# Kernel tuning notes

Hardware: AMD Instinct MI355X
Metric: run time of the kernel (lower is better)

Reference implementation:

```python
import jax, jax.numpy as jnp
import numpy as np

B, T, D, C = 16, 2048, 512, 20
K_EASY, K_HARD = 40, 20
M_BIG, M_SMALL = 7, 3
A4 = A5 = A6 = A7 = 1.0
EPS = 1e-05
DROP_P = 0.6


def setup_inputs() -> dict:
    key = jax.random.key(0)
    ks = jax.random.split(key, 6)
    attn = jax.random.uniform(ks[0], (B, T, 1), dtype=jnp.float32)
    mu = jax.random.normal(ks[1], (B, T, D), dtype=jnp.float32)
    var = jax.random.uniform(ks[2], (B, T, D), dtype=jnp.float32) * 0.9 + 0.1
    mu_clip = jax.random.normal(ks[3], (B, T, D), dtype=jnp.float32)
    text_feat = jax.random.normal(ks[4], (C, D), dtype=jnp.float32)
    keep = (jax.random.uniform(ks[5], (B, T)) >= DROP_P).astype(jnp.float32)
    drop_mask = keep / (1.0 - DROP_P)  # inverted-dropout mask on a ones tensor
    return dict(attn=attn, mu=mu, var=var, mu_clip=mu_clip, text_feat=text_feat, drop_mask=drop_mask)


def _normalize(x, axis=-1):
    n = jnp.linalg.norm(x, axis=axis, keepdims=True)
    return x / jnp.maximum(n, 1e-12)


def _select_topk(scores, emb, k):
    # torch: sort desc, take first k indices, gather along time dim
    _, idx = jax.lax.top_k(scores, k)  # [B,k]
    return jnp.take_along_axis(emb, idx[:, :, None], axis=1)  # [B,k,D]


def _window_reduce(x, w, op_min):
    # binary erosion/dilation along time with structure ones((1,w)), border_value=0
    lo, hi = w // 2, w - 1 - w // 2
    xp = jnp.pad(x, ((0, 0), (lo, hi)), constant_values=0.0)
    if op_min:
        return jax.lax.reduce_window(xp, jnp.inf, jax.lax.min, (1, w), (1, 1), 'VALID')
    return jax.lax.reduce_window(xp, -jnp.inf, jax.lax.max, (1, w), (1, 1), 'VALID')


def _kl_distance(mu_p, cov_p, mu_q, cov_q):
    # vectorized over all (i in k_p) x (j in k_q) pairs
    cov_p = cov_p + EPS
    cov_q = cov_q + EPS
    d = mu_p.shape[-1]
    diff = mu_q[:, None, :, :] - mu_p[:, :, None, :]        # [B,kp,kq,D]
    term1 = 0.5 * jnp.sum(diff * diff / cov_q[:, None, :, :], axis=-1)
    term2 = 0.5 * (jnp.sum(jnp.log(cov_q), -1)[:, None, :] - jnp.sum(jnp.log(cov_p), -1)[:, :, None])
    term3 = 0.5 * jnp.sum(cov_p[:, :, None, :] / cov_q[:, None, :, :], axis=-1)
    dist = term1 + term2 + term3 - 0.5 * d
    return jnp.mean(1.0 / (dist + 1.0), axis=(1, 2))        # [B]


def _prob_contrastive(hard_q, easy_pos, easy_neg):
    pos = _kl_distance(hard_q[0], hard_q[1], easy_pos[0], easy_pos[1])
    neg = _kl_distance(hard_q[0], hard_q[1], easy_neg[0], easy_neg[1])
    return jnp.mean(-(jnp.log(pos) + jnp.log(1.0 - neg)))


def _forward(attn, mu, var, mu_clip, text_feat, drop_mask):
    a = attn[..., 0]                                        # [B,T]
    a_drop = a * drop_mask
    a_rev = jnp.max(a, axis=1, keepdims=True) - a
    a_rev_drop = a_rev * drop_mask
    easy_act = (_select_topk(a_drop, mu, K_EASY), _select_topk(a_drop, var, K_EASY))
    easy_bkg = (_select_topk(a_rev_drop, mu, K_EASY), _select_topk(a_rev_drop, var, K_EASY))

    med = jnp.median(a, axis=1, keepdims=True)
    abin = jnp.where(a > med, 1.0, 0.0)
    er_M = _window_reduce(abin, M_BIG, True)
    er_m = _window_reduce(abin, M_SMALL, True)
    inner = jax.lax.stop_gradient(er_m - er_M)              # mask computed on detached numpy in torch
    dl_m = _window_reduce(abin, M_SMALL, False)
    dl_M = _window_reduce(abin, M_BIG, False)
    outer = jax.lax.stop_gradient(dl_M - dl_m)
    a_inner = a * inner
    a_outer = a * outer
    hard_act = (_select_topk(a_inner, mu, K_HARD), _select_topk(a_inner, var, K_HARD))
    hard_bkg = (_select_topk(a_outer, mu, K_HARD), _select_topk(a_outer, var, K_HARD))

    # Distillation
    sim = jnp.einsum('btd,btd->bt', _normalize(mu), _normalize(mu_clip))
    distill = A4 * (-jnp.log(jnp.mean((sim + 1.0) / 2.0)))

    act_loss = A5 * _prob_contrastive(hard_act, easy_act, easy_bkg)
    bkg_loss = A6 * _prob_contrastive(hard_bkg, easy_bkg, easy_act)

    emb = _normalize(text_feat)
    sim_m = emb @ jax.lax.stop_gradient(emb.T) - jnp.eye(emb.shape[0], dtype=emb.dtype)
    ortho = A7 * jnp.linalg.norm(sim_m)

    total = distill + act_loss + bkg_loss + ortho
    return total, distill, act_loss, bkg_loss, ortho


def reference(attn, mu, var, mu_clip, text_feat, drop_mask):
    return _forward(attn, mu, var, mu_clip, text_feat, drop_mask)
```

## Files before the change

kernel.cpp:

```cpp
#include <hip/hip_runtime.h>
#include <math.h>


#define BB 16
#define TT 2048
#define DD 512
#define CC 20
#define KEASY 40
#define KHARD 20
#define EPSF 1e-5f

typedef unsigned long long u64;

template <int CTRL>
__device__ __forceinline__ float dpp_mov(float x) {
  return __int_as_float(__builtin_amdgcn_update_dpp(
      0, __float_as_int(x), CTRL, 0xF, 0xF, true));
}
__device__ __forceinline__ float wsum63(float v) {
  v += dpp_mov<0x111>(v);
  v += dpp_mov<0x112>(v);
  v += dpp_mov<0x114>(v);
  v += dpp_mov<0x118>(v);
  v += dpp_mov<0x142>(v);
  v += dpp_mov<0x143>(v);
  return v;
}
__device__ __forceinline__ float wsum_bc(float v) {
  return __int_as_float(__builtin_amdgcn_readlane(__float_as_int(wsum63(v)), 63));
}
__device__ __forceinline__ float wmax_bc(float v) {
  v = fmaxf(v, dpp_mov<0x111>(v));
  v = fmaxf(v, dpp_mov<0x112>(v));
  v = fmaxf(v, dpp_mov<0x114>(v));
  v = fmaxf(v, dpp_mov<0x118>(v));
  v = fmaxf(v, dpp_mov<0x142>(v));
  v = fmaxf(v, dpp_mov<0x143>(v));
  return __int_as_float(__builtin_amdgcn_readlane(__float_as_int(v), 63));
}

__device__ __forceinline__ float kth_val(const float (&v)[32], unsigned k, unsigned hi) {
  unsigned lo = 0;
  while (lo < hi) {
    const unsigned mid = lo + ((hi - lo + 1) >> 1);
    const float mf = __uint_as_float(mid);
    unsigned c = 0;
#pragma unroll
    for (int r = 0; r < 32; r++) c += (unsigned)__popcll(__ballot(v[r] >= mf));
    if (c >= k) lo = mid; else hi = mid - 1;
  }
  return __uint_as_float(lo);
}

__global__ __launch_bounds__(256) void k_main1(const float* __restrict__ attn,
                                               const float* __restrict__ drop,
                                               const float* __restrict__ mu,
                                               const float* __restrict__ muc,
                                               const float* __restrict__ var,
                                               int* __restrict__ idxb,
                                               float* __restrict__ slogb,
                                               float* __restrict__ part,
                                               double* __restrict__ acc) {
  const int tid = threadIdx.x, wid = tid >> 6, lane = tid & 63;

  if (blockIdx.x >= 64) {
    __shared__ float s_red[4];
    const int blk = blockIdx.x - 64;
    const float* pmu = mu + (size_t)(blk * 4 + wid) * DD + lane * 4;
    const float* pmc = muc + (size_t)(blk * 4 + wid) * DD + lane * 4;
    float4 xa = *(const float4*)(pmu);
    float4 xb = *(const float4*)(pmu + 256);
    float4 ya = *(const float4*)(pmc);
    float4 yb = *(const float4*)(pmc + 256);
    float wacc = 0.f;
#pragma unroll
    for (int it = 0; it < 4; it++) {
      const float4 cxa = xa, cxb = xb, cya = ya, cyb = yb;
      if (it < 3) {
        const size_t off = (size_t)(it + 1) * 8192 * DD;
        xa = *(const float4*)(pmu + off);
        xb = *(const float4*)(pmu + off + 256);
        ya = *(const float4*)(pmc + off);
        yb = *(const float4*)(pmc + off + 256);
      }
      float dot = 0.f, n1 = 0.f, n2 = 0.f;
      dot = fmaf(cxa.x, cya.x, fmaf(cxa.y, cya.y, fmaf(cxa.z, cya.z, fmaf(cxa.w, cya.w, dot))));
      n1 = fmaf(cxa.x, cxa.x, fmaf(cxa.y, cxa.y, fmaf(cxa.z, cxa.z, fmaf(cxa.w, cxa.w, n1))));
      n2 = fmaf(cya.x, cya.x, fmaf(cya.y, cya.y, fmaf(cya.z, cya.z, fmaf(cya.w, cya.w, n2))));
      dot = fmaf(cxb.x, cyb.x, fmaf(cxb.y, cyb.y, fmaf(cxb.z, cyb.z, fmaf(cxb.w, cyb.w, dot))));
      n1 = fmaf(cxb.x, cxb.x, fmaf(cxb.y, cxb.y, fmaf(cxb.z, cxb.z, fmaf(cxb.w, cxb.w, n1))));
      n2 = fmaf(cyb.x, cyb.x, fmaf(cyb.y, cyb.y, fmaf(cyb.z, cyb.z, fmaf(cyb.w, cyb.w, n2))));
      dot = wsum63(dot);
      n1 = wsum63(n1);
      n2 = wsum63(n2);
      if (lane == 63) {
        const float sim = dot / (fmaxf(sqrtf(n1), 1e-12f) * fmaxf(sqrtf(n2), 1e-12f));
        wacc += (sim + 1.0f) * 0.5f;
      }
    }
    if (lane == 63) s_red[wid] = wacc;
    __syncthreads();
    if (tid == 0) part[blk] = s_red[0] + s_red[1] + s_red[2] + s_red[3];
    return;
  }

  __shared__ float s_a[TT];
  __shared__ int s_idx[KEASY];
  const int b = blockIdx.x >> 2, sel = blockIdx.x & 3;
  for (int i = tid; i < TT; i += 256) s_a[i] = attn[b * TT + i];
  __syncthreads();

  if (tid < 64) {
    if (blockIdx.x == 0) acc[lane] = 0.0;
    float v[32];
    float med = 0.f, mx = 0.f;
    if (sel >= 2) {
#pragma unroll
      for (int r = 0; r < 32; r++) v[r] = s_a[r * 64 + lane];
      const float v1 = kth_val(v, 1024, 0x3F800000u);
      const float v2 = kth_val(v, 1025, __float_as_uint(v1));
      med = 0.5f * (v1 + v2);
    }
    if (sel == 1) {
      float m = 0.f;
#pragma unroll
      for (int r = 0; r < 32; r++) m = fmaxf(m, s_a[r * 64 + lane]);
      mx = wmax_bc(m);
    }
#pragma unroll
    for (int r = 0; r < 32; r++) {
      const int i = r * 64 + lane;
      const float a = s_a[i];
      float score;
      if (sel == 0) {
        score = a * drop[b * TT + i];
      } else if (sel == 1) {
        score = (mx - a) * drop[b * TT + i];
      } else {
        bool sall = true, ball = true, sany = false, bany = false;
#pragma unroll
        for (int o = -3; o <= 3; o++) {
          const int t = i + o;
          const bool one = (t >= 0 && t < TT) ? (s_a[t] > med) : false;
          if (o >= -1 && o <= 1) { sall = sall && one; sany = sany || one; }
          ball = ball && one;
          bany = bany || one;
        }
        score = (sel == 2) ? ((sall && !ball) ? a : 0.f)
                           : ((bany && !sany) ? a : 0.f);
      }
      v[r] = score;
    }
    const unsigned K = (sel < 2) ? KEASY : KHARD;
    const unsigned hiS = (sel < 2) ? 0x40200000u : 0x3F800000u;
    const float ss = kth_val(v, K, hiS);
    unsigned cgt = 0;
#pragma unroll
    for (int r = 0; r < 32; r++) cgt += (unsigned)__popcll(__ballot(v[r] > ss));
    unsigned need = K - cgt;
    unsigned base = 0;
    const u64 lmask = (1ull << lane) - 1;
    int* dst = idxb + sel * (BB * KEASY) + b * KEASY;
#pragma unroll
    for (int r = 0; r < 32; r++) {
      const bool gt = v[r] > ss;
      const bool eq = v[r] == ss;
      const u64 beq = __ballot(eq);
      const unsigned neq = (unsigned)__popcll(beq);
      const unsigned take = (need < neq) ? need : neq;
      const bool tk = eq && ((unsigned)__popcll(beq & lmask) < take);
      const u64 bsel = __ballot(gt || tk);
      if (gt || tk) {
        const unsigned pos = base + (unsigned)__popcll(bsel & lmask);
        dst[pos] = r * 64 + lane;
        s_idx[pos] = r * 64 + lane;
      }
      base += (unsigned)__popcll(bsel);
      need -= take;
    }
  }
  __syncthreads();

  const int Ksel = (sel < 2) ? KEASY : KHARD;
  for (int j = wid; j < Ksel; j += 4) {
    const int t = s_idx[j];
    const float* row = var + ((size_t)b * TT + t) * DD;
    float a2 = 0.f;
#pragma unroll
    for (int c = 0; c < 2; c++) {
      float4 vv = *(const float4*)(row + c * 256 + lane * 4);
      a2 += __logf(vv.x + EPSF) + __logf(vv.y + EPSF) +
            __logf(vv.z + EPSF) + __logf(vv.w + EPSF);
    }
    a2 = wsum63(a2);
    if (lane == 63) slogb[sel * 640 + b * 40 + j] = a2;
  }
}

__global__ __launch_bounds__(256) void k_kl(const float* __restrict__ mu,
                                            const float* __restrict__ var,
                                            const int* __restrict__ idxb,
                                            const float* __restrict__ slogb,
                                            double* __restrict__ acc) {
  __shared__ __align__(16) float s_mup[DD];
  __shared__ __align__(16) float s_cvp[DD];
  __shared__ float s_red[4];
  const int blk = blockIdx.x;
  const int klid = blk / 320, rem = blk % 320, b = rem / 20, ip = rem % 20;
  const int psel = (klid < 2) ? 2 : 3;
  const int qsel = (klid == 0) ? 0 : (klid == 1) ? 1 : (klid == 2) ? 1 : 0;
  const int tid = threadIdx.x, wid = tid >> 6, lane = tid & 63;
  const int pidx = idxb[psel * 640 + b * 40 + ip];
  const float slog_p = slogb[psel * 640 + b * 40 + ip];
  const size_t pbase = ((size_t)b * TT + pidx) * DD;
  for (int i = tid; i < DD; i += 256) {
    s_mup[i] = mu[pbase + i];
    s_cvp[i] = var[pbase + i] + EPSF;
  }
  __syncthreads();
  float wacc = 0.f;
#pragma unroll
  for (int t = 0; t < 5; t++) {
    const int iqA = wid + 8 * t, iqB = iqA + 4;
    const int qA = idxb[qsel * 640 + b * 40 + iqA];
    const int qB = idxb[qsel * 640 + b * 40 + iqB];
    const float slqA = slogb[qsel * 640 + b * 40 + iqA];
    const float slqB = slogb[qsel * 640 + b * 40 + iqB];
    const size_t baA = ((size_t)b * TT + qA) * DD;
    const size_t baB = ((size_t)b * TT + qB) * DD;
    float a1A = 0.f, a3A = 0.f, a1B = 0.f, a3B = 0.f;
#pragma unroll
    for (int c = 0; c < 2; c++) {
      const int d0 = c * 256 + lane * 4;
      const float4 mqA = *(const float4*)(mu + baA + d0);
      const float4 vqA = *(const float4*)(var + baA + d0);
      const float4 mqB = *(const float4*)(mu + baB + d0);
      const float4 vqB = *(const float4*)(var + baB + d0);
      const float4 mp = *(const float4*)(&s_mup[d0]);
      const float4 cp = *(const float4*)(&s_cvp[d0]);
      { float r = 1.0f / (vqA.x + EPSF); float df = mqA.x - mp.x; a1A += df * df * r; a3A += cp.x * r; }
      { float r = 1.0f / (vqA.y + EPSF); float df = mqA.y - mp.y; a1A += df * df * r; a3A += cp.y * r; }
      { float r = 1.0f / (vqA.z + EPSF); float df = mqA.z - mp.z; a1A += df * df * r; a3A += cp.z * r; }
      { float r = 1.0f / (vqA.w + EPSF); float df = mqA.w - mp.w; a1A += df * df * r; a3A += cp.w * r; }
      { float r = 1.0f / (vqB.x + EPSF); float df = mqB.x - mp.x; a1B += df * df * r; a3B += cp.x * r; }
      { float r = 1.0f / (vqB.y + EPSF); float df = mqB.y - mp.y; a1B += df * df * r; a3B += cp.y * r; }
      { float r = 1.0f / (vqB.z + EPSF); float df = mqB.z - mp.z; a1B += df * df * r; a3B += cp.z * r; }
      { float r = 1.0f / (vqB.w + EPSF); float df = mqB.w - mp.w; a1B += df * df * r; a3B += cp.w * r; }
    }
    a1A = wsum63(a1A);
    a3A = wsum63(a3A);
    a1B = wsum63(a1B);
    a3B = wsum63(a3B);
    if (lane == 63) {
      const float dA = 0.5f * a1A + 0.5f * (slqA - slog_p) + 0.5f * a3A - 256.0f;
      const float dB = 0.5f * a1B + 0.5f * (slqB - slog_p) + 0.5f * a3B - 256.0f;
      wacc += 1.0f / (dA + 1.0f) + 1.0f / (dB + 1.0f);
    }
  }
  if (lane == 63) s_red[wid] = wacc;
  __syncthreads();
  if (tid == 0) {
    const double sum = (double)s_red[0] + s_red[1] + s_red[2] + s_red[3];
    atomicAdd(&acc[klid * 16 + b], sum);
  }
}

__global__ __launch_bounds__(256) void k_final(const float* __restrict__ text,
                                               const double* __restrict__ acc,
                                               const float* __restrict__ part,
                                               float* __restrict__ out) {
  __shared__ __align__(16) float s_e[CC * DD];
  __shared__ float s_red4[4];
  __shared__ double s_red[256];
  const int tid = threadIdx.x, wid = tid >> 6, lane = tid & 63;

  for (int r = wid; r < CC; r += 4) {
    float4 v[2];
    float ss = 0.f;
#pragma unroll
    for (int c = 0; c < 2; c++) {
      v[c] = *(const float4*)(text + r * DD + c * 256 + lane * 4);
      ss += v[c].x * v[c].x + v[c].y * v[c].y + v[c].z * v[c].z + v[c].w * v[c].w;
    }
    ss = wsum_bc(ss);
    const float n = fmaxf(sqrtf(ss), 1e-12f);
#pragma unroll
    for (int c = 0; c < 2; c++) {
      float4 w = v[c];
      w.x /= n; w.y /= n; w.z /= n; w.w /= n;
      *(float4*)(&s_e[r * DD + c * 256 + lane * 4]) = w;
    }
  }
  __syncthreads();
  float wss = 0.f;
  for (int p = wid; p < CC * CC; p += 4) {
    const int i = p / CC, j = p % CC;
    float dot = 0.f;
#pragma unroll
    for (int c = 0; c < 2; c++) {
      const int d0 = c * 256 + lane * 4;
      const float4 x = *(const float4*)(&s_e[i * DD + d0]);
      const float4 y = *(const float4*)(&s_e[j * DD + d0]);
      dot += x.x * y.x + x.y * y.y + x.z * y.z + x.w * y.w;
    }
    dot = wsum63(dot);
    if (lane == 63) {
      const float s = dot - (i == j ? 1.0f : 0.0f);
      wss += s * s;
    }
  }
  if (lane == 63) s_red4[wid] = wss;
  __syncthreads();

  double s = 0.0;
  for (int i = tid; i < 2048; i += 256) s += (double)part[i];
  s_red[tid] = s;
  __syncthreads();
  for (int st = 128; st; st >>= 1) {
    if (tid < st) s_red[tid] += s_red[tid + st];
    __syncthreads();
  }
  if (tid == 0) {
    const double distill = -log(s_red[0] / (double)(BB * TT));
    double act = 0.0, bkg = 0.0;
    for (int b = 0; b < 16; b++) {
      const double pa = acc[0 * 16 + b] / 800.0;
      const double na = acc[1 * 16 + b] / 800.0;
      const double pb = acc[2 * 16 + b] / 800.0;
      const double nb = acc[3 * 16 + b] / 800.0;
      act += -(log(pa) + log(1.0 - na));
      bkg += -(log(pb) + log(1.0 - nb));
    }
    act /= 16.0;
    bkg /= 16.0;
    const double ortho = sqrt((double)(s_red4[0] + s_red4[1] + s_red4[2] + s_red4[3]));
    const double total = distill + act + bkg + ortho;
    out[0] = (float)total;
    out[1] = (float)distill;
    out[2] = (float)act;
    out[3] = (float)bkg;
    out[4] = (float)ortho;
  }
}

extern "C" void kernel_launch(void* const* d_in, const int* in_sizes, int n_in,
                              void* d_out, int out_size, void* d_ws, size_t ws_size,
                              hipStream_t stream) {
  const float* attn = (const float*)d_in[0];
  const float* mu   = (const float*)d_in[1];
  const float* var  = (const float*)d_in[2];
  const float* muc  = (const float*)d_in[3];
  const float* text = (const float*)d_in[4];
  const float* drop = (const float*)d_in[5];
  float* out = (float*)d_out;

  double* acc  = (double*)d_ws;
  int* idxb    = (int*)(acc + 66);
  float* slogb = (float*)(idxb + 2560);
  float* part  = (float*)(slogb + 2560);

  k_main1<<<2112, 256, 0, stream>>>(attn, drop, mu, muc, var, idxb, slogb, part, acc);
  k_kl<<<1280, 256, 0, stream>>>(mu, var, idxb, slogb, acc);
  k_final<<<1, 256, 0, stream>>>(text, acc, part, out);
}
```

Baseline: 274.7 us.

## Restructure KL pairwise kernel with algebraic expansion and shared p-row caching

Replaces the 1280-block KL kernel with 64 blocks, one per (batch, loss term). Each block caches the 20 hard p-rows in shared memory as precomputed (mu^2+var+eps) and mu, then streams each q-row once with prefetching. The squared-difference term is expanded so each pair needs only two dot products against precomputed reciprocals. The per-row reductions that used to sit in the single final block (part sums, text orthogonality) move into extra parallel blocks, leaving a tiny finalize kernel. This cuts redundant global reads of q rows and removes the atomics, at the cost of far fewer blocks and longer serial per-block work plus some float cancellation risk from the expansion.

```diff
diff --git a/kernel.cpp b/kernel.cpp
--- a/kernel.cpp
+++ b/kernel.cpp
@@ -52,15 +52,15 @@
   return __uint_as_float(lo);
 }
 
-__global__ __launch_bounds__(256) void k_main1(const float* __restrict__ attn,
-                                               const float* __restrict__ drop,
-                                               const float* __restrict__ mu,
-                                               const float* __restrict__ muc,
-                                               const float* __restrict__ var,
-                                               int* __restrict__ idxb,
-                                               float* __restrict__ slogb,
-                                               float* __restrict__ part,
-                                               double* __restrict__ acc) {
+__global__ __launch_bounds__(256, 1) void k_main1(const float* __restrict__ attn,
+                                                  const float* __restrict__ drop,
+                                                  const float* __restrict__ mu,
+                                                  const float* __restrict__ muc,
+                                                  const float* __restrict__ var,
+                                                  int* __restrict__ idxb,
+                                                  float* __restrict__ slogb,
+                                                  float* __restrict__ part,
+                                                  double* __restrict__ acc) {
   const int tid = threadIdx.x, wid = tid >> 6, lane = tid & 63;
 
   if (blockIdx.x >= 64) {
@@ -111,7 +111,10 @@
   __syncthreads();
 
   if (tid < 64) {
-    if (blockIdx.x == 0) acc[lane] = 0.0;
+    if (blockIdx.x == 0) {
+      acc[lane] = 0.0;
+      if (lane < 2) acc[64 + lane] = 0.0;
+    }
     float v[32];
     float med = 0.f, mx = 0.f;
     if (sel >= 2) {
@@ -197,143 +200,182 @@
   }
 }
 
-__global__ __launch_bounds__(256) void k_kl(const float* __restrict__ mu,
-                                            const float* __restrict__ var,
-                                            const int* __restrict__ idxb,
-                                            const float* __restrict__ slogb,
-                                            double* __restrict__ acc) {
-  __shared__ __align__(16) float s_mup[DD];
-  __shared__ __align__(16) float s_cvp[DD];
-  __shared__ float s_red[4];
+__global__ __launch_bounds__(256, 1) void k_part2(const float* __restrict__ mu,
+                                                  const float* __restrict__ var,
+                                                  const int* __restrict__ idxb,
+                                                  const float* __restrict__ slogb,
+                                                  const float* __restrict__ part,
+                                                  const float* __restrict__ text,
+                                                  double* __restrict__ acc) {
+  __shared__ __align__(16) float smem[2 * KHARD * DD];
+  const int tid = threadIdx.x, wid = tid >> 6, lane = tid & 63;
   const int blk = blockIdx.x;
-  const int klid = blk / 320, rem = blk % 320, b = rem / 20, ip = rem % 20;
-  const int psel = (klid < 2) ? 2 : 3;
-  const int qsel = (klid == 0) ? 0 : (klid == 1) ? 1 : (klid == 2) ? 1 : 0;
-  const int tid = threadIdx.x, wid = tid >> 6, lane = tid & 63;
-  const int pidx = idxb[psel * 640 + b * 40 + ip];
-  const float slog_p = slogb[psel * 640 + b * 40 + ip];
-  const size_t pbase = ((size_t)b * TT + pidx) * DD;
-  for (int i = tid; i < DD; i += 256) {
-    s_mup[i] = mu[pbase + i];
-    s_cvp[i] = var[pbase + i] + EPSF;
-  }
-  __syncthreads();
-  float wacc = 0.f;
-#pragma unroll
-  for (int t = 0; t < 5; t++) {
-    const int iqA = wid + 8 * t, iqB = iqA + 4;
-    const int qA = idxb[qsel * 640 + b * 40 + iqA];
-    const int qB = idxb[qsel * 640 + b * 40 + iqB];
-    const float slqA = slogb[qsel * 640 + b * 40 + iqA];
-    const float slqB = slogb[qsel * 640 + b * 40 + iqB];
-    const size_t baA = ((size_t)b * TT + qA) * DD;
-    const size_t baB = ((size_t)b * TT + qB) * DD;
-    float a1A = 0.f, a3A = 0.f, a1B = 0.f, a3B = 0.f;
-#pragma unroll
-    for (int c = 0; c < 2; c++) {
-      const int d0 = c * 256 + lane * 4;
-      const float4 mqA = *(const float4*)(mu + baA + d0);
-      const float4 vqA = *(const float4*)(var + baA + d0);
-      const float4 mqB = *(const float4*)(mu + baB + d0);
-      const float4 vqB = *(const float4*)(var + baB + d0);
-      const float4 mp = *(const float4*)(&s_mup[d0]);
-      const float4 cp = *(const float4*)(&s_cvp[d0]);
-      { float r = 1.0f / (vqA.x + EPSF); float df = mqA.x - mp.x; a1A += df * df * r; a3A += cp.x * r; }
-      { float r = 1.0f / (vqA.y + EPSF); float df = mqA.y - mp.y; a1A += df * df * r; a3A += cp.y * r; }
-      { float r = 1.0f / (vqA.z + EPSF); float df = mqA.z - mp.z; a1A += df * df * r; a3A += cp.z * r; }
-      { float r = 1.0f / (vqA.w + EPSF); float df = mqA.w - mp.w; a1A += df * df * r; a3A += cp.w * r; }
-      { float r = 1.0f / (vqB.x + EPSF); float df = mqB.x - mp.x; a1B += df * df * r; a3B += cp.x * r; }
-      { float r = 1.0f / (vqB.y + EPSF); float df = mqB.y - mp.y; a1B += df * df * r; a3B += cp.y * r; }
-      { float r = 1.0f / (vqB.z + EPSF); float df = mqB.z - mp.z; a1B += df * df * r; a3B += cp.z * r; }
-      { float r = 1.0f / (vqB.w + EPSF); float df = mqB.w - mp.w; a1B += df * df * r; a3B += cp.w * r; }
-    }
-    a1A = wsum63(a1A);
-    a3A = wsum63(a3A);
-    a1B = wsum63(a1B);
-    a3B = wsum63(a3B);
-    if (lane == 63) {
-      const float dA = 0.5f * a1A + 0.5f * (slqA - slog_p) + 0.5f * a3A - 256.0f;
-      const float dB = 0.5f * a1B + 0.5f * (slqB - slog_p) + 0.5f * a3B - 256.0f;
-      wacc += 1.0f / (dA + 1.0f) + 1.0f / (dB + 1.0f);
-    }
-  }
-  if (lane == 63) s_red[wid] = wacc;
+
+  if (blk < 64) {
+    const int b = blk >> 2, klid = blk & 3;
+    const int psel = (klid < 2) ? 2 : 3;
+    const int qsel = (klid == 0 || klid == 3) ? 0 : 1;
+    float* sP1 = smem;
+    float* sP2 = smem + KHARD * DD;
+    __shared__ float sSlogP[KHARD];
+    __shared__ float s_out[4];
+    if (tid < KHARD) sSlogP[tid] = slogb[psel * 640 + b * 40 + tid];
+    for (int i = tid; i < KHARD * 128; i += 256) {
+      const int p = i >> 7, c = (i & 127) * 4;
+      const int t = idxb[psel * 640 + b * 40 + p];
+      const size_t base = ((size_t)b * TT + t) * DD + c;
+      const float4 m = *(const float4*)(mu + base);
+      const float4 vv = *(const float4*)(var + base);
+      float4 p1;
+      p1.x = fmaf(m.x, m.x, vv.x + EPSF);
+      p1.y = fmaf(m.y, m.y, vv.y + EPSF);
+      p1.z = fmaf(m.z, m.z, vv.z + EPSF);
+      p1.w = fmaf(m.w, m.w, vv.w + EPSF);
+      *(float4*)(sP1 + p * DD + c) = p1;
+      *(float4*)(sP2 + p * DD + c) = m;
+    }
+    __syncthreads();
+
+    const int d0 = lane * 4, d1 = 256 + lane * 4;
+    const int qbase_i = qsel * 640 + b * 40;
+    float wacc = 0.f;
+    int qidx = idxb[qbase_i + wid];
+    float slq = slogb[qbase_i + wid];
+    const float* qm = mu + ((size_t)b * TT + qidx) * DD;
+    const float* qv = var + ((size_t)b * TT + qidx) * DD;
+    float4 mqa = *(const float4*)(qm + d0);
+    float4 mqb = *(const float4*)(qm + d1);
+    float4 vqa = *(const float4*)(qv + d0);
+    float4 vqb = *(const float4*)(qv + d1);
+#pragma unroll 1
+    for (int t = 0; t < 10; t++) {
+      const float4 cma = mqa, cmb = mqb, cva = vqa, cvb = vqb;
+      const float cslq = slq;
+      if (t < 9) {
+        const int iqn = wid + 4 * (t + 1);
+        qidx = idxb[qbase_i + iqn];
+        slq = slogb[qbase_i + iqn];
+        const float* nm = mu + ((size_t)b * TT + qidx) * DD;
+        const float* nv = var + ((size_t)b * TT + qidx) * DD;
+        mqa = *(const float4*)(nm + d0);
+        mqb = *(const float4*)(nm + d1);
+        vqa = *(const float4*)(nv + d0);
+        vqb = *(const float4*)(nv + d1);
+      }
+      float4 ra, rb, qra, qrb;
+      ra.x = 1.0f / (cva.x + EPSF); ra.y = 1.0f / (cva.y + EPSF);
+      ra.z = 1.0f / (cva.z + EPSF); ra.w = 1.0f / (cva.w + EPSF);
+      rb.x = 1.0f / (cvb.x + EPSF); rb.y = 1.0f / (cvb.y + EPSF);
+      rb.z = 1.0f / (cvb.z + EPSF); rb.w = 1.0f / (cvb.w + EPSF);
+      qra.x = cma.x * ra.x; qra.y = cma.y * ra.y;
+      qra.z = cma.z * ra.z; qra.w = cma.w * ra.w;
+      qrb.x = cmb.x * rb.x; qrb.y = cmb.y * rb.y;
+      qrb.z = cmb.z * rb.z; qrb.w = cmb.w * rb.w;
+      float cqp = cma.x * qra.x + cma.y * qra.y + cma.z * qra.z + cma.w * qra.w +
+                  cmb.x * qrb.x + cmb.y * qrb.y + cmb.z * qrb.z + cmb.w * qrb.w;
+      const float cq = wsum63(cqp);
+      for (int p = 0; p < KHARD; p++) {
+        const float4 p1a = *(const float4*)(sP1 + p * DD + d0);
+        const float4 p1b = *(const float4*)(sP1 + p * DD + d1);
+        const float4 p2a = *(const float4*)(sP2 + p * DD + d0);
+        const float4 p2b = *(const float4*)(sP2 + p * DD + d1);
+        const float s1 = p1a.x * ra.x + p1a.y * ra.y + p1a.z * ra.z + p1a.w * ra.w +
+                         p1b.x * rb.x + p1b.y * rb.y + p1b.z * rb.z + p1b.w * rb.w;
+        const float s2 = p2a.x * qra.x + p2a.y * qra.y + p2a.z * qra.z + p2a.w * qra.w +
+                         p2b.x * qrb.x + p2b.y * qrb.y + p2b.z * qrb.z + p2b.w * qrb.w;
+        const float h = wsum63(fmaf(0.5f, s1, -s2));
+        if (lane == 63) {
+          const float dist = h + 0.5f * cq + 0.5f * cslq - 0.5f * sSlogP[p] - 256.0f;
+          wacc += 1.0f / (dist + 1.0f);
+        }
+      }
+    }
+    if (lane == 63) s_out[wid] = wacc;
+    __syncthreads();
+    if (tid == 0)
+      acc[klid * 16 + b] = (double)s_out[0] + s_out[1] + s_out[2] + s_out[3];
+    return;
+  }
+
+  if (blk == 64) {
+    double* sd = (double*)smem;
+    double s = 0.0;
+    for (int i = tid; i < 2048; i += 256) s += (double)part[i];
+    sd[tid] = s;
+    __syncthreads();
+    for (int st = 128; st; st >>= 1) {
+      if (tid < st) sd[tid] += sd[tid + st];
+      __syncthreads();
+    }
+    if (tid == 0) acc[64] = sd[0];
+    return;
+  }
+
+  {
+    float* s_e = smem;
+    __shared__ float s_red4[4];
+    for (int r = wid; r < CC; r += 4) {
+      float4 v[2];
+      float ss = 0.f;
+#pragma unroll
+      for (int c = 0; c < 2; c++) {
+        v[c] = *(const float4*)(text + r * DD + c * 256 + lane * 4);
+        ss += v[c].x * v[c].x + v[c].y * v[c].y + v[c].z * v[c].z + v[c].w * v[c].w;
+      }
+      ss = wsum_bc(ss);
+      const float n = fmaxf(sqrtf(ss), 1e-12f);
+#pragma unroll
+      for (int c = 0; c < 2; c++) {
+        float4 w = v[c];
+        w.x /= n; w.y /= n; w.z /= n; w.w /= n;
+        *(float4*)(s_e + r * DD + c * 256 + lane * 4) = w;
+      }
+    }
+    __syncthreads();
+    float wss = 0.f;
+    for (int p = wid; p < CC * CC; p += 4) {
+      const int i = p / CC, j = p % CC;
+      float dot = 0.f;
+#pragma unroll
+      for (int c = 0; c < 2; c++) {
+        const int d0 = c * 256 + lane * 4;
+        const float4 x = *(const float4*)(s_e + i * DD + d0);
+        const float4 y = *(const float4*)(s_e + j * DD + d0);
+        dot += x.x * y.x + x.y * y.y + x.z * y.z + x.w * y.w;
+      }
+      dot = wsum63(dot);
+      if (lane == 63) {
+        const float s = dot - (i == j ? 1.0f : 0.0f);
+        wss += s * s;
+      }
+    }
+    if (lane == 63) s_red4[wid] = wss;
+    __syncthreads();
+    if (tid == 0)
+      acc[65] = (double)(s_red4[0] + s_red4[1] + s_red4[2] + s_red4[3]);
+  }
+}
+
+__global__ __launch_bounds__(64) void k_final(const double* __restrict__ acc,
+                                              float* __restrict__ out) {
+  __shared__ double sla[16], slb[16];
+  const int tid = threadIdx.x;
+  if (tid < 16) {
+    const double pa = acc[0 * 16 + tid] / 800.0;
+    const double na = acc[1 * 16 + tid] / 800.0;
+    const double pb = acc[2 * 16 + tid] / 800.0;
+    const double nb = acc[3 * 16 + tid] / 800.0;
+    sla[tid] = -(log(pa) + log(1.0 - na));
+    slb[tid] = -(log(pb) + log(1.0 - nb));
+  }
   __syncthreads();
   if (tid == 0) {
-    const double sum = (double)s_red[0] + s_red[1] + s_red[2] + s_red[3];
-    atomicAdd(&acc[klid * 16 + b], sum);
-  }
-}
-
-__global__ __launch_bounds__(256) void k_final(const float* __restrict__ text,
-                                               const double* __restrict__ acc,
-                                               const float* __restrict__ part,
-                                               float* __restrict__ out) {
-  __shared__ __align__(16) float s_e[CC * DD];
-  __shared__ float s_red4[4];
-  __shared__ double s_red[256];
-  const int tid = threadIdx.x, wid = tid >> 6, lane = tid & 63;
-
-  for (int r = wid; r < CC; r += 4) {
-    float4 v[2];
-    float ss = 0.f;
-#pragma unroll
-    for (int c = 0; c < 2; c++) {
-      v[c] = *(const float4*)(text + r * DD + c * 256 + lane * 4);
-      ss += v[c].x * v[c].x + v[c].y * v[c].y + v[c].z * v[c].z + v[c].w * v[c].w;
-    }
-    ss = wsum_bc(ss);
-    const float n = fmaxf(sqrtf(ss), 1e-12f);
-#pragma unroll
-    for (int c = 0; c < 2; c++) {
-      float4 w = v[c];
-      w.x /= n; w.y /= n; w.z /= n; w.w /= n;
-      *(float4*)(&s_e[r * DD + c * 256 + lane * 4]) = w;
-    }
-  }
-  __syncthreads();
-  float wss = 0.f;
-  for (int p = wid; p < CC * CC; p += 4) {
-    const int i = p / CC, j = p % CC;
-    float dot = 0.f;
-#pragma unroll
-    for (int c = 0; c < 2; c++) {
-      const int d0 = c * 256 + lane * 4;
-      const float4 x = *(const float4*)(&s_e[i * DD + d0]);
-      const float4 y = *(const float4*)(&s_e[j * DD + d0]);
-      dot += x.x * y.x + x.y * y.y + x.z * y.z + x.w * y.w;
-    }
-    dot = wsum63(dot);
-    if (lane == 63) {
-      const float s = dot - (i == j ? 1.0f : 0.0f);
-      wss += s * s;
-    }
-  }
-  if (lane == 63) s_red4[wid] = wss;
-  __syncthreads();
-
-  double s = 0.0;
-  for (int i = tid; i < 2048; i += 256) s += (double)part[i];
-  s_red[tid] = s;
-  __syncthreads();
-  for (int st = 128; st; st >>= 1) {
-    if (tid < st) s_red[tid] += s_red[tid + st];
-    __syncthreads();
-  }
-  if (tid == 0) {
-    const double distill = -log(s_red[0] / (double)(BB * TT));
     double act = 0.0, bkg = 0.0;
-    for (int b = 0; b < 16; b++) {
-      const double pa = acc[0 * 16 + b] / 800.0;
-      const double na = acc[1 * 16 + b] / 800.0;
-      const double pb = acc[2 * 16 + b] / 800.0;
-      const double nb = acc[3 * 16 + b] / 800.0;
-      act += -(log(pa) + log(1.0 - na));
-      bkg += -(log(pb) + log(1.0 - nb));
-    }
+    for (int b = 0; b < 16; b++) { act += sla[b]; bkg += slb[b]; }
     act /= 16.0;
     bkg /= 16.0;
-    const double ortho = sqrt((double)(s_red4[0] + s_red4[1] + s_red4[2] + s_red4[3]));
+    const double distill = -log(acc[64] / (double)(BB * TT));
+    const double ortho = sqrt(acc[65]);
     const double total = distill + act + bkg + ortho;
     out[0] = (float)total;
     out[1] = (float)distill;
@@ -360,6 +402,6 @@
   float* part  = (float*)(slogb + 2560);
 
   k_main1<<<2112, 256, 0, stream>>>(attn, drop, mu, muc, var, idxb, slogb, part, acc);
-  k_kl<<<1280, 256, 0, stream>>>(mu, var, idxb, slogb, acc);
-  k_final<<<1, 256, 0, stream>>>(text, acc, part, out);
-}
+  k_part2<<<66, 256, 0, stream>>>(mu, var, idxb, slogb, part, text, acc);
+  k_final<<<1, 64, 0, stream>>>(acc, out);
+}
```

Result: no change. 269.8 us (-1.8%).
